# Performance work log

Hardware: AMD Instinct MI355X
Metric: run time of the kernel (lower is better)

## Reference

```python
import jax, jax.numpy as jnp
import numpy as np

N = 100_000          # nodes
E = 1_600_000        # edges (avg degree 16)
NODE_SCA, NODE_VEC = 4, 3
EDGE_SCA, EDGE_VEC = 6, 3
OUT_SCA, OUT_VEC = 16, 16
CUTOFF = 10.0
EPS = 1e-6
SLOPE_VN = 0.2       # VNLeakyReLU negative slope (SurfGen default)
SLOPE_SCA = 0.01     # nn.LeakyReLU default


def setup_inputs() -> dict:
    key = jax.random.key(0)
    ks = jax.random.split(key, 22)
    rn = lambda k, s: jax.random.normal(k, s, dtype=jnp.float32)
    return {
        # forward args
        'node_sca': rn(ks[0], (N, NODE_SCA)),
        'node_vec': rn(ks[1], (N, NODE_VEC, 3)),
        'edge_sca': rn(ks[2], (E, EDGE_SCA)),
        'edge_vec': rn(ks[3], (E, EDGE_VEC, 3)),
        'gds_dist': jax.random.uniform(ks[4], (E,), dtype=jnp.float32) * 12.0,
        'edge_index': jax.random.randint(ks[5], (2, E), 0, N),
        # message projections (Linear weights stored [in,out])
        'W_nss': rn(ks[6], (NODE_SCA, OUT_SCA)) * 0.3, 'b_nss': rn(ks[7], (OUT_SCA,)) * 0.1,
        'W_ess': rn(ks[8], (EDGE_SCA, OUT_SCA)) * 0.3, 'b_ess': rn(ks[9], (OUT_SCA,)) * 0.1,
        'W_nsv': rn(ks[10], (NODE_SCA, OUT_SCA)) * 0.3, 'b_nsv': rn(ks[11], (OUT_SCA,)) * 0.1,
        'W_esv': rn(ks[12], (EDGE_SCA, OUT_SCA)) * 0.3, 'b_esv': rn(ks[13], (OUT_SCA,)) * 0.1,
        'W_nvv': rn(ks[14], (NODE_VEC, OUT_VEC)) * 0.3,   # VNLinear (no bias)
        'W_evv': rn(ks[15], (EDGE_VEC, OUT_VEC)) * 0.3,
        # GVPerceptronVN(16,16,16,16): GVLinear (dim_hid = 16) + VN LeakyReLU
        'W_lv':  rn(ks[16], (OUT_VEC, OUT_VEC)) * 0.25,   # lin_vector   (no bias)
        'W_lv2': rn(ks[17], (OUT_VEC, OUT_VEC)) * 0.25,   # lin_vector2  (no bias)
        'W_ls':  rn(ks[18], (OUT_VEC + OUT_SCA, OUT_SCA)) * 0.25,  # lin_scalar (no bias)
        'W_gate': rn(ks[19], (OUT_SCA, OUT_VEC)) * 0.25, 'b_gate': rn(ks[20], (OUT_VEC,)) * 0.1,
        'W_dir': rn(ks[21], (OUT_VEC, OUT_VEC)) * 0.25,   # VNLeakyReLU direction (no bias)
    }


def vn_linear(x, W):
    # x: [n, c_in, 3], W: [c_in, c_out] -> [n, c_out, 3]
    return jnp.einsum('nci,co->noi', x, W)


def reference(node_sca, node_vec, edge_sca, edge_vec, gds_dist, edge_index,
              W_nss, b_nss, W_ess, b_ess, W_nsv, b_nsv, W_esv, b_esv,
              W_nvv, W_evv, W_lv, W_lv2, W_ls, W_gate, b_gate, W_dir):
    src = edge_index[0]
    num_nodes = node_sca.shape[0]

    # cosine cutoff coefficient
    coeff = 0.5 * (jnp.cos(gds_dist * (jnp.pi / CUTOFF)) + 1.0)
    coeff = coeff * (gds_dist <= CUTOFF) * (gds_dist >= 0.0)  # [E]

    # scalar message: gather node proj, mix with edge proj, cutoff-weight
    node_ss = node_sca @ W_nss + b_nss                          # [N,16]
    edge_ss = edge_sca @ W_ess + b_ess                          # [E,16]
    msg_sca = node_ss[src] * edge_ss * coeff[:, None]           # [E,16]

    # vector message
    node_vv = vn_linear(node_vec, W_nvv)                        # [N,16,3]
    edge_vv = vn_linear(edge_vec, W_evv)                        # [E,16,3]
    node_sv = node_sca @ W_nsv + b_nsv                          # [N,16]
    edge_sv = edge_sca @ W_esv + b_esv                          # [E,16]
    msg_vec = (node_vv[src] * edge_sv[:, :, None]
               + node_sv[src][:, :, None] * edge_vv) * coeff[:, None, None]  # [E,16,3]

    # scatter_sum into source nodes (matches original's edge_index[0])
    aggr_sca = jax.ops.segment_sum(msg_sca, src, num_segments=num_nodes)  # [N,16]
    aggr_vec = jax.ops.segment_sum(msg_vec, src, num_segments=num_nodes)  # [N,16,3]

    # --- GVPerceptronVN: GVLinear ---
    v_inter = vn_linear(aggr_vec, W_lv)                          # [N,16,3]
    v_norm = jnp.sqrt(jnp.sum(v_inter * v_inter, axis=-1))       # [N,16]
    out_sca = jnp.concatenate([v_norm, aggr_sca], axis=-1) @ W_ls  # [N,16]
    out_vec = vn_linear(v_inter, W_lv2)                          # [N,16,3]
    gate = jax.nn.sigmoid(out_sca @ W_gate + b_gate)[:, :, None]
    out_vec = gate * out_vec

    # --- VNLeakyReLU on vectors ---
    d = vn_linear(out_vec, W_dir)                                # [N,16,3]
    dot = jnp.sum(out_vec * d, axis=-1, keepdims=True)
    mask = (dot >= 0).astype(out_vec.dtype)
    d_norm_sq = jnp.sum(d * d, axis=-1, keepdims=True)
    out_vec = SLOPE_VN * out_vec + (1.0 - SLOPE_VN) * (
        mask * out_vec + (1.0 - mask) * (out_vec - (dot / (d_norm_sq + EPS)) * d))

    # LeakyReLU on scalars
    out_sca = jnp.where(out_sca >= 0, out_sca, SLOPE_SCA * out_sca)
    return out_sca, out_vec
```

## Files before the change

kernel.cpp:

```cpp
#include <hip/hip_runtime.h>
#include <hip/hip_fp16.h>
#include <math.h>

#define CUTOFF_F 10.0f
#define PI_OVER_CUTOFF 0.31415926535897931f
#define KCAP 32

__global__ __launch_bounds__(256) void bucket_scatter(
    const float* __restrict__ gds,
    const int* __restrict__ eidx,
    const float* __restrict__ edge_sca,
    const float* __restrict__ edge_vec,
    int* __restrict__ count,
    __half* __restrict__ bucket,
    float* __restrict__ aggr,
    int E)
{
    int e = blockIdx.x * 256 + threadIdx.x;
    if (e >= E) return;

    float d = gds[e];
    if (d < 0.0f || d > CUTOFF_F) return;

    float c = 0.5f * (__cosf(d * PI_OVER_CUTOFF) + 1.0f);
    int src = eidx[e];
    const float* es = edge_sca + (size_t)e * 6;
    const float* ev = edge_vec + (size_t)e * 9;

    float f[16];
#pragma unroll
    for (int i = 0; i < 6; ++i) f[i] = c * es[i];
    f[6] = c;
#pragma unroll
    for (int i = 0; i < 9; ++i) f[7 + i] = c * ev[i];

    int slot = atomicAdd(&count[src], 1);
    if (slot < KCAP) {
        union { __half h[16]; uint4 u[2]; } pk;
#pragma unroll
        for (int i = 0; i < 16; ++i) pk.h[i] = __float2half(f[i]);
        uint4* pb = (uint4*)(bucket + ((size_t)src * KCAP + slot) * 16);
        pb[0] = pk.u[0];
        pb[1] = pk.u[1];
    } else {
        float* base = aggr + (size_t)src * 16;
#pragma unroll
        for (int i = 0; i < 16; ++i) atomicAdd(base + i, f[i]);
    }
}

__global__ __launch_bounds__(256) void edge_aggregate(
    const float* __restrict__ edge_sca, const float* __restrict__ edge_vec,
    const float* __restrict__ gds, const int* __restrict__ eidx,
    float* __restrict__ aggr, int E)
{
    int e = blockIdx.x * blockDim.x + threadIdx.x;
    if (e >= E) return;
    int src = eidx[e];
    float d = gds[e];
    float coeff = 0.0f;
    if (d >= 0.0f && d <= CUTOFF_F)
        coeff = 0.5f * (__cosf(d * PI_OVER_CUTOFF) + 1.0f);
    float* base = aggr + (size_t)src * 16;
    const float* es = edge_sca + (size_t)e * 6;
    const float* ev = edge_vec + (size_t)e * 9;
#pragma unroll
    for (int c = 0; c < 6; ++c) atomicAdd(base + c, coeff * es[c]);
    atomicAdd(base + 6, coeff);
#pragma unroll
    for (int k = 0; k < 9; ++k) atomicAdd(base + 7 + k, coeff * ev[k]);
}

__global__ __launch_bounds__(256) void node_fused(
    const float* __restrict__ node_sca,
    const float* __restrict__ node_vec,
    const int* __restrict__ count,
    const __half* __restrict__ payload,
    const float* __restrict__ aggr,
    const float* __restrict__ W_nss, const float* __restrict__ b_nss,
    const float* __restrict__ W_ess, const float* __restrict__ b_ess,
    const float* __restrict__ W_nsv, const float* __restrict__ b_nsv,
    const float* __restrict__ W_esv, const float* __restrict__ b_esv,
    const float* __restrict__ W_nvv, const float* __restrict__ W_evv,
    const float* __restrict__ W_lv,  const float* __restrict__ W_lv2,
    const float* __restrict__ W_ls,
    const float* __restrict__ W_gate, const float* __restrict__ b_gate,
    const float* __restrict__ W_dir,
    float* __restrict__ out,
    int N, int mode)
{
    __shared__ float sW_nss[64],  sb_nss[16];
    __shared__ float sW_ess[96],  sb_ess[16];
    __shared__ float sW_nsv[64],  sb_nsv[16];
    __shared__ float sW_esv[96],  sb_esv[16];
    __shared__ float sW_nvv[48],  sW_evv[48];
    __shared__ float sW_lv[256],  sW_lv2[256];
    __shared__ float sW_ls[512];
    __shared__ float sW_gate[256], sb_gate[16];
    __shared__ float sW_dir[256];

    __shared__ float s_in  [16 * 33];
    __shared__ float s_avec[16 * 49];
    __shared__ float s_cat [16 * 33];
    __shared__ float s_vint[16 * 49];
    __shared__ float s_osca[16 * 17];
    __shared__ float s_ovec[16 * 49];

    const int t = threadIdx.x;
    {
        for (int i = t; i < 64;  i += 256) { sW_nss[i] = W_nss[i]; sW_nsv[i] = W_nsv[i]; }
        for (int i = t; i < 96;  i += 256) { sW_ess[i] = W_ess[i]; sW_esv[i] = W_esv[i]; }
        for (int i = t; i < 48;  i += 256) { sW_nvv[i] = W_nvv[i]; sW_evv[i] = W_evv[i]; }
        for (int i = t; i < 256; i += 256) {
            sW_lv[i]   = W_lv[i];
            sW_lv2[i]  = W_lv2[i];
            sW_gate[i] = W_gate[i];
            sW_dir[i]  = W_dir[i];
        }
        for (int i = t; i < 512; i += 256) sW_ls[i] = W_ls[i];
        if (t < 16) {
            sb_nss[t]  = b_nss[t];
            sb_ess[t]  = b_ess[t];
            sb_nsv[t]  = b_nsv[t];
            sb_esv[t]  = b_esv[t];
            sb_gate[t] = b_gate[t];
        }
    }

    const int slot = t >> 4;
    const int o    = t & 15;
    const int n    = blockIdx.x * 16 + slot;
    const bool valid = (n < N);

    if (valid) {
        if (o < 4) s_in[slot * 33 + o]     = node_sca[(size_t)n * 4 + o];
        if (o < 9) s_in[slot * 33 + 4 + o] = node_vec[(size_t)n * 9 + o];
    }

    if (mode == 1) {
        float acc[8] = {0.f, 0.f, 0.f, 0.f, 0.f, 0.f, 0.f, 0.f};
        const int h  = o & 1;
        const int sg = o >> 1;
        if (valid) {
            int cnt = count[n];
            if (cnt > KCAP) cnt = KCAP;
            const uint4* pu = (const uint4*)payload + (size_t)n * (KCAP * 2);
#pragma unroll
            for (int k = 0; k < 4; ++k) {
                int s = sg + 8 * k;
                if (s < cnt) {
                    uint4 v = pu[o + 16 * k];
                    const __half2* hp = (const __half2*)&v;
#pragma unroll
                    for (int j = 0; j < 4; ++j) {
                        float2 f2 = __half22float2(hp[j]);
                        acc[2 * j]     += f2.x;
                        acc[2 * j + 1] += f2.y;
                    }
                }
            }
        }
#pragma unroll
        for (int m = 2; m <= 8; m <<= 1) {
#pragma unroll
            for (int j = 0; j < 8; ++j)
                acc[j] += __shfl_xor(acc[j], m, 16);
        }
        if (valid && o < 2) {
#pragma unroll
            for (int j = 0; j < 8; ++j)
                s_in[slot * 33 + 13 + 8 * h + j] =
                    acc[j] + aggr[(size_t)n * 16 + 8 * h + j];
        }
    } else {
        if (valid) s_in[slot * 33 + 13 + o] = aggr[(size_t)n * 16 + o];
    }
    __syncthreads();

    const float* in = s_in + slot * 33;

    float nss = sb_nss[o], nsv = sb_nsv[o];
#pragma unroll
    for (int c = 0; c < 4; ++c) {
        float x = in[c];
        nss += x * sW_nss[c * 16 + o];
        nsv += x * sW_nsv[c * 16 + o];
    }
    float nvv0 = 0.f, nvv1 = 0.f, nvv2 = 0.f;
#pragma unroll
    for (int c = 0; c < 3; ++c) {
        float w = sW_nvv[c * 16 + o];
        nvv0 += in[4 + c * 3 + 0] * w;
        nvv1 += in[4 + c * 3 + 1] * w;
        nvv2 += in[4 + c * 3 + 2] * w;
    }
    float cc = in[19];
    float es = cc * sb_ess[o], ev = cc * sb_esv[o];
#pragma unroll
    for (int c = 0; c < 6; ++c) {
        float a = in[13 + c];
        es += a * sW_ess[c * 16 + o];
        ev += a * sW_esv[c * 16 + o];
    }
    float EV0 = 0.f, EV1 = 0.f, EV2 = 0.f;
#pragma unroll
    for (int c = 0; c < 3; ++c) {
        float w = sW_evv[c * 16 + o];
        EV0 += in[20 + c * 3 + 0] * w;
        EV1 += in[20 + c * 3 + 1] * w;
        EV2 += in[20 + c * 3 + 2] * w;
    }

    float asca = nss * es;
    float av0 = nvv0 * ev + nsv * EV0;
    float av1 = nvv1 * ev + nsv * EV1;
    float av2 = nvv2 * ev + nsv * EV2;
    s_avec[slot * 49 + o * 3 + 0] = av0;
    s_avec[slot * 49 + o * 3 + 1] = av1;
    s_avec[slot * 49 + o * 3 + 2] = av2;
    s_cat[slot * 33 + 16 + o] = asca;
    __syncthreads();

    float vi0 = 0.f, vi1 = 0.f, vi2 = 0.f;
#pragma unroll
    for (int c = 0; c < 16; ++c) {
        float w = sW_lv[c * 16 + o];
        const float* a = &s_avec[slot * 49 + c * 3];
        vi0 += a[0] * w; vi1 += a[1] * w; vi2 += a[2] * w;
    }
    float vnorm = sqrtf(vi0 * vi0 + vi1 * vi1 + vi2 * vi2);
    s_vint[slot * 49 + o * 3 + 0] = vi0;
    s_vint[slot * 49 + o * 3 + 1] = vi1;
    s_vint[slot * 49 + o * 3 + 2] = vi2;
    s_cat[slot * 33 + o] = vnorm;
    __syncthreads();

    float osca = 0.f;
#pragma unroll
    for (int c = 0; c < 32; ++c)
        osca += s_cat[slot * 33 + c] * sW_ls[c * 16 + o];
    float ov0 = 0.f, ov1 = 0.f, ov2 = 0.f;
#pragma unroll
    for (int c = 0; c < 16; ++c) {
        float w = sW_lv2[c * 16 + o];
        const float* a = &s_vint[slot * 49 + c * 3];
        ov0 += a[0] * w; ov1 += a[1] * w; ov2 += a[2] * w;
    }
    s_osca[slot * 17 + o] = osca;
    __syncthreads();

    float g = sb_gate[o];
#pragma unroll
    for (int c = 0; c < 16; ++c)
        g += s_osca[slot * 17 + c] * sW_gate[c * 16 + o];
    g = 1.0f / (1.0f + __expf(-g));
    ov0 *= g; ov1 *= g; ov2 *= g;
    s_ovec[slot * 49 + o * 3 + 0] = ov0;
    s_ovec[slot * 49 + o * 3 + 1] = ov1;
    s_ovec[slot * 49 + o * 3 + 2] = ov2;
    __syncthreads();

    float dv0 = 0.f, dv1 = 0.f, dv2 = 0.f;
#pragma unroll
    for (int c = 0; c < 16; ++c) {
        float w = sW_dir[c * 16 + o];
        const float* a = &s_ovec[slot * 49 + c * 3];
        dv0 += a[0] * w; dv1 += a[1] * w; dv2 += a[2] * w;
    }
    float dot = ov0 * dv0 + ov1 * dv1 + ov2 * dv2;
    if (dot < 0.0f) {
        float dn = dv0 * dv0 + dv1 * dv1 + dv2 * dv2;
        float f = 0.8f * dot / (dn + 1e-6f);
        ov0 -= f * dv0; ov1 -= f * dv1; ov2 -= f * dv2;
    }

    if (valid) {
        float so = (osca >= 0.0f) ? osca : 0.01f * osca;
        out[(size_t)n * 16 + o] = so;
        size_t vb = (size_t)N * 16 + (size_t)n * 48 + (size_t)o * 3;
        out[vb + 0] = ov0;
        out[vb + 1] = ov1;
        out[vb + 2] = ov2;
    }
}

extern "C" void kernel_launch(void* const* d_in, const int* in_sizes, int n_in,
                              void* d_out, int out_size, void* d_ws, size_t ws_size,
                              hipStream_t stream)
{
    const float* node_sca = (const float*)d_in[0];
    const float* node_vec = (const float*)d_in[1];
    const float* edge_sca = (const float*)d_in[2];
    const float* edge_vec = (const float*)d_in[3];
    const float* gds      = (const float*)d_in[4];
    const int*   eidx     = (const int*)d_in[5];

    const int N = in_sizes[0] / 4;
    const int E = in_sizes[4];

    int*    count  = (int*)d_ws;
    float*  aggr   = (float*)(count + N);
    __half* bucket = (__half*)(aggr + (size_t)N * 16);
    size_t  hdr    = (size_t)N * 4 + (size_t)N * 64;
    size_t  need   = hdr + (size_t)N * KCAP * 16 * sizeof(__half);

    if (ws_size >= need) {
        hipMemsetAsync(count, 0, hdr, stream);
        bucket_scatter<<<(E + 255) / 256, 256, 0, stream>>>(
            gds, eidx, edge_sca, edge_vec, count, bucket, aggr, E);
        node_fused<<<(N + 15) / 16, 256, 0, stream>>>(
            node_sca, node_vec, count, bucket, aggr,
            (const float*)d_in[6],  (const float*)d_in[7],
            (const float*)d_in[8],  (const float*)d_in[9],
            (const float*)d_in[10], (const float*)d_in[11],
            (const float*)d_in[12], (const float*)d_in[13],
            (const float*)d_in[14], (const float*)d_in[15],
            (const float*)d_in[16], (const float*)d_in[17],
            (const float*)d_in[18],
            (const float*)d_in[19], (const float*)d_in[20],
            (const float*)d_in[21],
            (float*)d_out, N, 1);
        return;
    }

    size_t zb = hdr;
    if (zb > ws_size) zb = ws_size;
    hipMemsetAsync(count, 0, zb, stream);
    edge_aggregate<<<(E + 255) / 256, 256, 0, stream>>>(
        edge_sca, edge_vec, gds, eidx, aggr, E);
    node_fused<<<(N + 15) / 16, 256, 0, stream>>>(
        node_sca, node_vec, count, bucket, aggr,
        (const float*)d_in[6],  (const float*)d_in[7],
        (const float*)d_in[8],  (const float*)d_in[9],
        (const float*)d_in[10], (const float*)d_in[11],
        (const float*)d_in[12], (const float*)d_in[13],
        (const float*)d_in[14], (const float*)d_in[15],
        (const float*)d_in[16], (const float*)d_in[17],
        (const float*)d_in[18],
        (const float*)d_in[19], (const float*)d_in[20],
        (const float*)d_in[21],
        (float*)d_out, N, 0);
}
```

Measured before the change: 289.1 us.

## Fuse memset, edge scatter and node stage into one cooperative kernel

Replaces the memset, edge bucket-scatter kernel and node kernel with a single cooperative kernel launched on 1024 blocks. The phases are separated by grid-wide syncs, and the loops are grid-strided over edges and node tiles. The aim is to remove launch and inter-kernel gap overhead and to load the weights into shared memory only once per block. In exchange, a fixed grid size may limit parallelism in the scatter phase, and grid syncs add their own cost. If the cooperative launch fails, the code falls back to the previous path.

```diff
diff --git a/kernel.cpp b/kernel.cpp
--- a/kernel.cpp
+++ b/kernel.cpp
@@ -1,10 +1,271 @@
 #include <hip/hip_runtime.h>
+#include <hip/hip_cooperative_groups.h>
 #include <hip/hip_fp16.h>
 #include <math.h>
+
+namespace cg = cooperative_groups;
 
 #define CUTOFF_F 10.0f
 #define PI_OVER_CUTOFF 0.31415926535897931f
 #define KCAP 32
+
+__global__ __launch_bounds__(256) void fused_all(
+    const float* __restrict__ node_sca,
+    const float* __restrict__ node_vec,
+    const float* __restrict__ edge_sca,
+    const float* __restrict__ edge_vec,
+    const float* __restrict__ gds,
+    const int* __restrict__ eidx,
+    int* __restrict__ count,
+    __half* __restrict__ bucket,
+    float* __restrict__ aggr,
+    const float* __restrict__ W_nss, const float* __restrict__ b_nss,
+    const float* __restrict__ W_ess, const float* __restrict__ b_ess,
+    const float* __restrict__ W_nsv, const float* __restrict__ b_nsv,
+    const float* __restrict__ W_esv, const float* __restrict__ b_esv,
+    const float* __restrict__ W_nvv, const float* __restrict__ W_evv,
+    const float* __restrict__ W_lv,  const float* __restrict__ W_lv2,
+    const float* __restrict__ W_ls,
+    const float* __restrict__ W_gate, const float* __restrict__ b_gate,
+    const float* __restrict__ W_dir,
+    float* __restrict__ out,
+    int N, int E)
+{
+    __shared__ float sW_nss[64],  sb_nss[16];
+    __shared__ float sW_ess[96],  sb_ess[16];
+    __shared__ float sW_nsv[64],  sb_nsv[16];
+    __shared__ float sW_esv[96],  sb_esv[16];
+    __shared__ float sW_nvv[48],  sW_evv[48];
+    __shared__ float sW_lv[256],  sW_lv2[256];
+    __shared__ float sW_ls[512];
+    __shared__ float sW_gate[256], sb_gate[16];
+    __shared__ float sW_dir[256];
+
+    __shared__ float s_in  [16 * 33];
+    __shared__ float s_avec[16 * 49];
+    __shared__ float s_cat [16 * 33];
+    __shared__ float s_vint[16 * 49];
+    __shared__ float s_osca[16 * 17];
+    __shared__ float s_ovec[16 * 49];
+
+    const int t = threadIdx.x;
+    {
+        for (int i = t; i < 64;  i += 256) { sW_nss[i] = W_nss[i]; sW_nsv[i] = W_nsv[i]; }
+        for (int i = t; i < 96;  i += 256) { sW_ess[i] = W_ess[i]; sW_esv[i] = W_esv[i]; }
+        for (int i = t; i < 48;  i += 256) { sW_nvv[i] = W_nvv[i]; sW_evv[i] = W_evv[i]; }
+        for (int i = t; i < 256; i += 256) {
+            sW_lv[i]   = W_lv[i];
+            sW_lv2[i]  = W_lv2[i];
+            sW_gate[i] = W_gate[i];
+            sW_dir[i]  = W_dir[i];
+        }
+        for (int i = t; i < 512; i += 256) sW_ls[i] = W_ls[i];
+        if (t < 16) {
+            sb_nss[t]  = b_nss[t];
+            sb_ess[t]  = b_ess[t];
+            sb_nsv[t]  = b_nsv[t];
+            sb_esv[t]  = b_esv[t];
+            sb_gate[t] = b_gate[t];
+        }
+    }
+
+    {
+        int* z = count;
+        const int total = N * 17;
+        for (int i = blockIdx.x * 256 + t; i < total; i += gridDim.x * 256)
+            z[i] = 0;
+    }
+    cg::this_grid().sync();
+
+    for (int e = blockIdx.x * 256 + t; e < E; e += gridDim.x * 256) {
+        float d = gds[e];
+        if (d < 0.0f || d > CUTOFF_F) continue;
+
+        float c = 0.5f * (__cosf(d * PI_OVER_CUTOFF) + 1.0f);
+        int src = eidx[e];
+        const float* es = edge_sca + (size_t)e * 6;
+        const float* ev = edge_vec + (size_t)e * 9;
+
+        float f[16];
+#pragma unroll
+        for (int i = 0; i < 6; ++i) f[i] = c * es[i];
+        f[6] = c;
+#pragma unroll
+        for (int i = 0; i < 9; ++i) f[7 + i] = c * ev[i];
+
+        int sl = atomicAdd(&count[src], 1);
+        if (sl < KCAP) {
+            union { __half h[16]; uint4 u[2]; } pk;
+#pragma unroll
+            for (int i = 0; i < 16; ++i) pk.h[i] = __float2half(f[i]);
+            uint4* pb = (uint4*)(bucket + ((size_t)src * KCAP + sl) * 16);
+            pb[0] = pk.u[0];
+            pb[1] = pk.u[1];
+        } else {
+            float* base = aggr + (size_t)src * 16;
+#pragma unroll
+            for (int i = 0; i < 16; ++i) atomicAdd(base + i, f[i]);
+        }
+    }
+    cg::this_grid().sync();
+
+    const int slot = t >> 4;
+    const int o    = t & 15;
+    const int h    = o & 1;
+    const int sg   = o >> 1;
+    const int nTiles = (N + 15) / 16;
+
+    for (int tile = blockIdx.x; tile < nTiles; tile += gridDim.x) {
+        const int n = tile * 16 + slot;
+        const bool valid = (n < N);
+
+        if (valid) {
+            if (o < 4) s_in[slot * 33 + o]     = node_sca[(size_t)n * 4 + o];
+            if (o < 9) s_in[slot * 33 + 4 + o] = node_vec[(size_t)n * 9 + o];
+        }
+
+        float acc[8] = {0.f, 0.f, 0.f, 0.f, 0.f, 0.f, 0.f, 0.f};
+        if (valid) {
+            int cnt = count[n];
+            if (cnt > KCAP) cnt = KCAP;
+            const uint4* pu = (const uint4*)bucket + (size_t)n * (KCAP * 2);
+#pragma unroll
+            for (int k = 0; k < 4; ++k) {
+                int s = sg + 8 * k;
+                if (s < cnt) {
+                    uint4 v = pu[o + 16 * k];
+                    const __half2* hp = (const __half2*)&v;
+#pragma unroll
+                    for (int j = 0; j < 4; ++j) {
+                        float2 f2 = __half22float2(hp[j]);
+                        acc[2 * j]     += f2.x;
+                        acc[2 * j + 1] += f2.y;
+                    }
+                }
+            }
+        }
+#pragma unroll
+        for (int m = 2; m <= 8; m <<= 1) {
+#pragma unroll
+            for (int j = 0; j < 8; ++j)
+                acc[j] += __shfl_xor(acc[j], m, 16);
+        }
+        if (valid && o < 2) {
+#pragma unroll
+            for (int j = 0; j < 8; ++j)
+                s_in[slot * 33 + 13 + 8 * h + j] =
+                    acc[j] + aggr[(size_t)n * 16 + 8 * h + j];
+        }
+        __syncthreads();
+
+        const float* in = s_in + slot * 33;
+
+        float nss = sb_nss[o], nsv = sb_nsv[o];
+#pragma unroll
+        for (int c = 0; c < 4; ++c) {
+            float x = in[c];
+            nss += x * sW_nss[c * 16 + o];
+            nsv += x * sW_nsv[c * 16 + o];
+        }
+        float nvv0 = 0.f, nvv1 = 0.f, nvv2 = 0.f;
+#pragma unroll
+        for (int c = 0; c < 3; ++c) {
+            float w = sW_nvv[c * 16 + o];
+            nvv0 += in[4 + c * 3 + 0] * w;
+            nvv1 += in[4 + c * 3 + 1] * w;
+            nvv2 += in[4 + c * 3 + 2] * w;
+        }
+        float cc = in[19];
+        float es = cc * sb_ess[o], ev = cc * sb_esv[o];
+#pragma unroll
+        for (int c = 0; c < 6; ++c) {
+            float a = in[13 + c];
+            es += a * sW_ess[c * 16 + o];
+            ev += a * sW_esv[c * 16 + o];
+        }
+        float EV0 = 0.f, EV1 = 0.f, EV2 = 0.f;
+#pragma unroll
+        for (int c = 0; c < 3; ++c) {
+            float w = sW_evv[c * 16 + o];
+            EV0 += in[20 + c * 3 + 0] * w;
+            EV1 += in[20 + c * 3 + 1] * w;
+            EV2 += in[20 + c * 3 + 2] * w;
+        }
+
+        float asca = nss * es;
+        float av0 = nvv0 * ev + nsv * EV0;
+        float av1 = nvv1 * ev + nsv * EV1;
+        float av2 = nvv2 * ev + nsv * EV2;
+        s_avec[slot * 49 + o * 3 + 0] = av0;
+        s_avec[slot * 49 + o * 3 + 1] = av1;
+        s_avec[slot * 49 + o * 3 + 2] = av2;
+        s_cat[slot * 33 + 16 + o] = asca;
+        __syncthreads();
+
+        float vi0 = 0.f, vi1 = 0.f, vi2 = 0.f;
+#pragma unroll
+        for (int c = 0; c < 16; ++c) {
+            float w = sW_lv[c * 16 + o];
+            const float* a = &s_avec[slot * 49 + c * 3];
+            vi0 += a[0] * w; vi1 += a[1] * w; vi2 += a[2] * w;
+        }
+        float vnorm = sqrtf(vi0 * vi0 + vi1 * vi1 + vi2 * vi2);
+        s_vint[slot * 49 + o * 3 + 0] = vi0;
+        s_vint[slot * 49 + o * 3 + 1] = vi1;
+        s_vint[slot * 49 + o * 3 + 2] = vi2;
+        s_cat[slot * 33 + o] = vnorm;
+        __syncthreads();
+
+        float osca = 0.f;
+#pragma unroll
+        for (int c = 0; c < 32; ++c)
+            osca += s_cat[slot * 33 + c] * sW_ls[c * 16 + o];
+        float ov0 = 0.f, ov1 = 0.f, ov2 = 0.f;
+#pragma unroll
+        for (int c = 0; c < 16; ++c) {
+            float w = sW_lv2[c * 16 + o];
+            const float* a = &s_vint[slot * 49 + c * 3];
+            ov0 += a[0] * w; ov1 += a[1] * w; ov2 += a[2] * w;
+        }
+        s_osca[slot * 17 + o] = osca;
+        __syncthreads();
+
+        float g = sb_gate[o];
+#pragma unroll
+        for (int c = 0; c < 16; ++c)
+            g += s_osca[slot * 17 + c] * sW_gate[c * 16 + o];
+        g = 1.0f / (1.0f + __expf(-g));
+        ov0 *= g; ov1 *= g; ov2 *= g;
+        s_ovec[slot * 49 + o * 3 + 0] = ov0;
+        s_ovec[slot * 49 + o * 3 + 1] = ov1;
+        s_ovec[slot * 49 + o * 3 + 2] = ov2;
+        __syncthreads();
+
+        float dv0 = 0.f, dv1 = 0.f, dv2 = 0.f;
+#pragma unroll
+        for (int c = 0; c < 16; ++c) {
+            float w = sW_dir[c * 16 + o];
+            const float* a = &s_ovec[slot * 49 + c * 3];
+            dv0 += a[0] * w; dv1 += a[1] * w; dv2 += a[2] * w;
+        }
+        float dot = ov0 * dv0 + ov1 * dv1 + ov2 * dv2;
+        if (dot < 0.0f) {
+            float dn = dv0 * dv0 + dv1 * dv1 + dv2 * dv2;
+            float fr = 0.8f * dot / (dn + 1e-6f);
+            ov0 -= fr * dv0; ov1 -= fr * dv1; ov2 -= fr * dv2;
+        }
+
+        if (valid) {
+            float so = (osca >= 0.0f) ? osca : 0.01f * osca;
+            out[(size_t)n * 16 + o] = so;
+            size_t vb = (size_t)N * 16 + (size_t)n * 48 + (size_t)o * 3;
+            out[vb + 0] = ov0;
+            out[vb + 1] = ov1;
+            out[vb + 2] = ov2;
+        }
+        __syncthreads();
+    }
+}
 
 __global__ __launch_bounds__(256) void bucket_scatter(
     const float* __restrict__ gds,
@@ -305,6 +566,40 @@
     size_t  need   = hdr + (size_t)N * KCAP * 16 * sizeof(__half);
 
     if (ws_size >= need) {
+        const float* p_Wnss = (const float*)d_in[6];
+        const float* p_bnss = (const float*)d_in[7];
+        const float* p_Wess = (const float*)d_in[8];
+        const float* p_bess = (const float*)d_in[9];
+        const float* p_Wnsv = (const float*)d_in[10];
+        const float* p_bnsv = (const float*)d_in[11];
+        const float* p_Wesv = (const float*)d_in[12];
+        const float* p_besv = (const float*)d_in[13];
+        const float* p_Wnvv = (const float*)d_in[14];
+        const float* p_Wevv = (const float*)d_in[15];
+        const float* p_Wlv  = (const float*)d_in[16];
+        const float* p_Wlv2 = (const float*)d_in[17];
+        const float* p_Wls  = (const float*)d_in[18];
+        const float* p_Wgt  = (const float*)d_in[19];
+        const float* p_bgt  = (const float*)d_in[20];
+        const float* p_Wdir = (const float*)d_in[21];
+        float* p_out = (float*)d_out;
+        int nN = N, nE = E;
+
+        void* kargs[] = {
+            (void*)&node_sca, (void*)&node_vec, (void*)&edge_sca,
+            (void*)&edge_vec, (void*)&gds, (void*)&eidx,
+            (void*)&count, (void*)&bucket, (void*)&aggr,
+            (void*)&p_Wnss, (void*)&p_bnss, (void*)&p_Wess, (void*)&p_bess,
+            (void*)&p_Wnsv, (void*)&p_bnsv, (void*)&p_Wesv, (void*)&p_besv,
+            (void*)&p_Wnvv, (void*)&p_Wevv, (void*)&p_Wlv, (void*)&p_Wlv2,
+            (void*)&p_Wls, (void*)&p_Wgt, (void*)&p_bgt, (void*)&p_Wdir,
+            (void*)&p_out, (void*)&nN, (void*)&nE
+        };
+
+        hipError_t err = hipLaunchCooperativeKernel(
+            (const void*)fused_all, dim3(1024), dim3(256), kargs, 0, stream);
+        if (err == hipSuccess) return;
+
         hipMemsetAsync(count, 0, hdr, stream);
         bucket_scatter<<<(E + 255) / 256, 256, 0, stream>>>(
             gds, eidx, edge_sca, edge_vec, count, bucket, aggr, E);
```

Measured after the change: 532.2 us. 1.84x slower.

## Add overflow flag, nontemporal bucket stores, and persistent node kernel grid

Applied to the files above, without the earlier changes.

The scatter kernel now writes bucket entries with nontemporal stores and sets a global flag whenever any node exceeds its bucket capacity. The node kernel reads that flag once per block and skips reading the dense aggregate array when no overflow happened. The node kernel also becomes a grid-stride loop over a fixed number of blocks, so shared-memory weight staging is paid once per block rather than once per 16 nodes. The risks are an extra barrier per tile iteration and possibly lower occupancy from the capped grid.

```diff
diff --git a/kernel.cpp b/kernel.cpp
--- a/kernel.cpp
+++ b/kernel.cpp
@@ -5,6 +5,8 @@
 #define CUTOFF_F 10.0f
 #define PI_OVER_CUTOFF 0.31415926535897931f
 #define KCAP 32
+
+typedef unsigned int uint32x4 __attribute__((ext_vector_type(4)));
 
 __global__ __launch_bounds__(256) void bucket_scatter(
     const float* __restrict__ gds,
@@ -12,6 +14,7 @@
     const float* __restrict__ edge_sca,
     const float* __restrict__ edge_vec,
     int* __restrict__ count,
+    int* __restrict__ flag,
     __half* __restrict__ bucket,
     float* __restrict__ aggr,
     int E)
@@ -36,13 +39,14 @@
 
     int slot = atomicAdd(&count[src], 1);
     if (slot < KCAP) {
-        union { __half h[16]; uint4 u[2]; } pk;
+        union { __half h[16]; uint32x4 u[2]; } pk;
 #pragma unroll
         for (int i = 0; i < 16; ++i) pk.h[i] = __float2half(f[i]);
-        uint4* pb = (uint4*)(bucket + ((size_t)src * KCAP + slot) * 16);
-        pb[0] = pk.u[0];
-        pb[1] = pk.u[1];
+        uint32x4* pb = (uint32x4*)(bucket + ((size_t)src * KCAP + slot) * 16);
+        __builtin_nontemporal_store(pk.u[0], pb);
+        __builtin_nontemporal_store(pk.u[1], pb + 1);
     } else {
+        flag[0] = 1;
         float* base = aggr + (size_t)src * 16;
 #pragma unroll
         for (int i = 0; i < 16; ++i) atomicAdd(base + i, f[i]);
@@ -75,6 +79,7 @@
     const float* __restrict__ node_sca,
     const float* __restrict__ node_vec,
     const int* __restrict__ count,
+    const int* __restrict__ flag,
     const __half* __restrict__ payload,
     const float* __restrict__ aggr,
     const float* __restrict__ W_nss, const float* __restrict__ b_nss,
@@ -105,6 +110,7 @@
     __shared__ float s_vint[16 * 49];
     __shared__ float s_osca[16 * 17];
     __shared__ float s_ovec[16 * 49];
+    __shared__ int   s_flag;
 
     const int t = threadIdx.x;
     {
@@ -125,162 +131,176 @@
             sb_esv[t]  = b_esv[t];
             sb_gate[t] = b_gate[t];
         }
+        if (t == 0) s_flag = flag[0];
     }
+    __syncthreads();
 
     const int slot = t >> 4;
     const int o    = t & 15;
-    const int n    = blockIdx.x * 16 + slot;
-    const bool valid = (n < N);
-
-    if (valid) {
-        if (o < 4) s_in[slot * 33 + o]     = node_sca[(size_t)n * 4 + o];
-        if (o < 9) s_in[slot * 33 + 4 + o] = node_vec[(size_t)n * 9 + o];
-    }
-
-    if (mode == 1) {
-        float acc[8] = {0.f, 0.f, 0.f, 0.f, 0.f, 0.f, 0.f, 0.f};
-        const int h  = o & 1;
-        const int sg = o >> 1;
+    const int h    = o & 1;
+    const int sg   = o >> 1;
+    const int useOvf = s_flag;
+    const int nTiles = (N + 15) / 16;
+
+    for (int tile = blockIdx.x; tile < nTiles; tile += gridDim.x) {
+        const int n = tile * 16 + slot;
+        const bool valid = (n < N);
+
         if (valid) {
-            int cnt = count[n];
-            if (cnt > KCAP) cnt = KCAP;
-            const uint4* pu = (const uint4*)payload + (size_t)n * (KCAP * 2);
-#pragma unroll
-            for (int k = 0; k < 4; ++k) {
-                int s = sg + 8 * k;
-                if (s < cnt) {
-                    uint4 v = pu[o + 16 * k];
-                    const __half2* hp = (const __half2*)&v;
-#pragma unroll
-                    for (int j = 0; j < 4; ++j) {
-                        float2 f2 = __half22float2(hp[j]);
-                        acc[2 * j]     += f2.x;
-                        acc[2 * j + 1] += f2.y;
+            if (o < 4) s_in[slot * 33 + o]     = node_sca[(size_t)n * 4 + o];
+            if (o < 9) s_in[slot * 33 + 4 + o] = node_vec[(size_t)n * 9 + o];
+        }
+
+        if (mode == 1) {
+            float acc[8] = {0.f, 0.f, 0.f, 0.f, 0.f, 0.f, 0.f, 0.f};
+            if (valid) {
+                int cnt = count[n];
+                if (cnt > KCAP) cnt = KCAP;
+                const uint4* pu = (const uint4*)payload + (size_t)n * (KCAP * 2);
+#pragma unroll
+                for (int k = 0; k < 4; ++k) {
+                    int s = sg + 8 * k;
+                    if (s < cnt) {
+                        uint4 v = pu[o + 16 * k];
+                        const __half2* hp = (const __half2*)&v;
+#pragma unroll
+                        for (int j = 0; j < 4; ++j) {
+                            float2 f2 = __half22float2(hp[j]);
+                            acc[2 * j]     += f2.x;
+                            acc[2 * j + 1] += f2.y;
+                        }
                     }
                 }
             }
-        }
-#pragma unroll
-        for (int m = 2; m <= 8; m <<= 1) {
-#pragma unroll
-            for (int j = 0; j < 8; ++j)
-                acc[j] += __shfl_xor(acc[j], m, 16);
-        }
-        if (valid && o < 2) {
-#pragma unroll
-            for (int j = 0; j < 8; ++j)
-                s_in[slot * 33 + 13 + 8 * h + j] =
-                    acc[j] + aggr[(size_t)n * 16 + 8 * h + j];
-        }
-    } else {
-        if (valid) s_in[slot * 33 + 13 + o] = aggr[(size_t)n * 16 + o];
-    }
-    __syncthreads();
-
-    const float* in = s_in + slot * 33;
-
-    float nss = sb_nss[o], nsv = sb_nsv[o];
-#pragma unroll
-    for (int c = 0; c < 4; ++c) {
-        float x = in[c];
-        nss += x * sW_nss[c * 16 + o];
-        nsv += x * sW_nsv[c * 16 + o];
-    }
-    float nvv0 = 0.f, nvv1 = 0.f, nvv2 = 0.f;
-#pragma unroll
-    for (int c = 0; c < 3; ++c) {
-        float w = sW_nvv[c * 16 + o];
-        nvv0 += in[4 + c * 3 + 0] * w;
-        nvv1 += in[4 + c * 3 + 1] * w;
-        nvv2 += in[4 + c * 3 + 2] * w;
-    }
-    float cc = in[19];
-    float es = cc * sb_ess[o], ev = cc * sb_esv[o];
-#pragma unroll
-    for (int c = 0; c < 6; ++c) {
-        float a = in[13 + c];
-        es += a * sW_ess[c * 16 + o];
-        ev += a * sW_esv[c * 16 + o];
-    }
-    float EV0 = 0.f, EV1 = 0.f, EV2 = 0.f;
-#pragma unroll
-    for (int c = 0; c < 3; ++c) {
-        float w = sW_evv[c * 16 + o];
-        EV0 += in[20 + c * 3 + 0] * w;
-        EV1 += in[20 + c * 3 + 1] * w;
-        EV2 += in[20 + c * 3 + 2] * w;
-    }
-
-    float asca = nss * es;
-    float av0 = nvv0 * ev + nsv * EV0;
-    float av1 = nvv1 * ev + nsv * EV1;
-    float av2 = nvv2 * ev + nsv * EV2;
-    s_avec[slot * 49 + o * 3 + 0] = av0;
-    s_avec[slot * 49 + o * 3 + 1] = av1;
-    s_avec[slot * 49 + o * 3 + 2] = av2;
-    s_cat[slot * 33 + 16 + o] = asca;
-    __syncthreads();
-
-    float vi0 = 0.f, vi1 = 0.f, vi2 = 0.f;
-#pragma unroll
-    for (int c = 0; c < 16; ++c) {
-        float w = sW_lv[c * 16 + o];
-        const float* a = &s_avec[slot * 49 + c * 3];
-        vi0 += a[0] * w; vi1 += a[1] * w; vi2 += a[2] * w;
-    }
-    float vnorm = sqrtf(vi0 * vi0 + vi1 * vi1 + vi2 * vi2);
-    s_vint[slot * 49 + o * 3 + 0] = vi0;
-    s_vint[slot * 49 + o * 3 + 1] = vi1;
-    s_vint[slot * 49 + o * 3 + 2] = vi2;
-    s_cat[slot * 33 + o] = vnorm;
-    __syncthreads();
-
-    float osca = 0.f;
-#pragma unroll
-    for (int c = 0; c < 32; ++c)
-        osca += s_cat[slot * 33 + c] * sW_ls[c * 16 + o];
-    float ov0 = 0.f, ov1 = 0.f, ov2 = 0.f;
-#pragma unroll
-    for (int c = 0; c < 16; ++c) {
-        float w = sW_lv2[c * 16 + o];
-        const float* a = &s_vint[slot * 49 + c * 3];
-        ov0 += a[0] * w; ov1 += a[1] * w; ov2 += a[2] * w;
-    }
-    s_osca[slot * 17 + o] = osca;
-    __syncthreads();
-
-    float g = sb_gate[o];
-#pragma unroll
-    for (int c = 0; c < 16; ++c)
-        g += s_osca[slot * 17 + c] * sW_gate[c * 16 + o];
-    g = 1.0f / (1.0f + __expf(-g));
-    ov0 *= g; ov1 *= g; ov2 *= g;
-    s_ovec[slot * 49 + o * 3 + 0] = ov0;
-    s_ovec[slot * 49 + o * 3 + 1] = ov1;
-    s_ovec[slot * 49 + o * 3 + 2] = ov2;
-    __syncthreads();
-
-    float dv0 = 0.f, dv1 = 0.f, dv2 = 0.f;
-#pragma unroll
-    for (int c = 0; c < 16; ++c) {
-        float w = sW_dir[c * 16 + o];
-        const float* a = &s_ovec[slot * 49 + c * 3];
-        dv0 += a[0] * w; dv1 += a[1] * w; dv2 += a[2] * w;
-    }
-    float dot = ov0 * dv0 + ov1 * dv1 + ov2 * dv2;
-    if (dot < 0.0f) {
-        float dn = dv0 * dv0 + dv1 * dv1 + dv2 * dv2;
-        float f = 0.8f * dot / (dn + 1e-6f);
-        ov0 -= f * dv0; ov1 -= f * dv1; ov2 -= f * dv2;
-    }
-
-    if (valid) {
-        float so = (osca >= 0.0f) ? osca : 0.01f * osca;
-        out[(size_t)n * 16 + o] = so;
-        size_t vb = (size_t)N * 16 + (size_t)n * 48 + (size_t)o * 3;
-        out[vb + 0] = ov0;
-        out[vb + 1] = ov1;
-        out[vb + 2] = ov2;
+#pragma unroll
+            for (int m = 2; m <= 8; m <<= 1) {
+#pragma unroll
+                for (int j = 0; j < 8; ++j)
+                    acc[j] += __shfl_xor(acc[j], m, 16);
+            }
+            if (valid && o < 2) {
+                if (useOvf) {
+#pragma unroll
+                    for (int j = 0; j < 8; ++j)
+                        s_in[slot * 33 + 13 + 8 * h + j] =
+                            acc[j] + aggr[(size_t)n * 16 + 8 * h + j];
+                } else {
+#pragma unroll
+                    for (int j = 0; j < 8; ++j)
+                        s_in[slot * 33 + 13 + 8 * h + j] = acc[j];
+                }
+            }
+        } else {
+            if (valid) s_in[slot * 33 + 13 + o] = aggr[(size_t)n * 16 + o];
+        }
+        __syncthreads();
+
+        const float* in = s_in + slot * 33;
+
+        float nss = sb_nss[o], nsv = sb_nsv[o];
+#pragma unroll
+        for (int c = 0; c < 4; ++c) {
+            float x = in[c];
+            nss += x * sW_nss[c * 16 + o];
+            nsv += x * sW_nsv[c * 16 + o];
+        }
+        float nvv0 = 0.f, nvv1 = 0.f, nvv2 = 0.f;
+#pragma unroll
+        for (int c = 0; c < 3; ++c) {
+            float w = sW_nvv[c * 16 + o];
+            nvv0 += in[4 + c * 3 + 0] * w;
+            nvv1 += in[4 + c * 3 + 1] * w;
+            nvv2 += in[4 + c * 3 + 2] * w;
+        }
+        float cc = in[19];
+        float es = cc * sb_ess[o], ev = cc * sb_esv[o];
+#pragma unroll
+        for (int c = 0; c < 6; ++c) {
+            float a = in[13 + c];
+            es += a * sW_ess[c * 16 + o];
+            ev += a * sW_esv[c * 16 + o];
+        }
+        float EV0 = 0.f, EV1 = 0.f, EV2 = 0.f;
+#pragma unroll
+        for (int c = 0; c < 3; ++c) {
+            float w = sW_evv[c * 16 + o];
+            EV0 += in[20 + c * 3 + 0] * w;
+            EV1 += in[20 + c * 3 + 1] * w;
+            EV2 += in[20 + c * 3 + 2] * w;
+        }
+
+        float asca = nss * es;
+        float av0 = nvv0 * ev + nsv * EV0;
+        float av1 = nvv1 * ev + nsv * EV1;
+        float av2 = nvv2 * ev + nsv * EV2;
+        s_avec[slot * 49 + o * 3 + 0] = av0;
+        s_avec[slot * 49 + o * 3 + 1] = av1;
+        s_avec[slot * 49 + o * 3 + 2] = av2;
+        s_cat[slot * 33 + 16 + o] = asca;
+        __syncthreads();
+
+        float vi0 = 0.f, vi1 = 0.f, vi2 = 0.f;
+#pragma unroll
+        for (int c = 0; c < 16; ++c) {
+            float w = sW_lv[c * 16 + o];
+            const float* a = &s_avec[slot * 49 + c * 3];
+            vi0 += a[0] * w; vi1 += a[1] * w; vi2 += a[2] * w;
+        }
+        float vnorm = sqrtf(vi0 * vi0 + vi1 * vi1 + vi2 * vi2);
+        s_vint[slot * 49 + o * 3 + 0] = vi0;
+        s_vint[slot * 49 + o * 3 + 1] = vi1;
+        s_vint[slot * 49 + o * 3 + 2] = vi2;
+        s_cat[slot * 33 + o] = vnorm;
+        __syncthreads();
+
+        float osca = 0.f;
+#pragma unroll
+        for (int c = 0; c < 32; ++c)
+            osca += s_cat[slot * 33 + c] * sW_ls[c * 16 + o];
+        float ov0 = 0.f, ov1 = 0.f, ov2 = 0.f;
+#pragma unroll
+        for (int c = 0; c < 16; ++c) {
+            float w = sW_lv2[c * 16 + o];
+            const float* a = &s_vint[slot * 49 + c * 3];
+            ov0 += a[0] * w; ov1 += a[1] * w; ov2 += a[2] * w;
+        }
+        s_osca[slot * 17 + o] = osca;
+        __syncthreads();
+
+        float g = sb_gate[o];
+#pragma unroll
+        for (int c = 0; c < 16; ++c)
+            g += s_osca[slot * 17 + c] * sW_gate[c * 16 + o];
+        g = 1.0f / (1.0f + __expf(-g));
+        ov0 *= g; ov1 *= g; ov2 *= g;
+        s_ovec[slot * 49 + o * 3 + 0] = ov0;
+        s_ovec[slot * 49 + o * 3 + 1] = ov1;
+        s_ovec[slot * 49 + o * 3 + 2] = ov2;
+        __syncthreads();
+
+        float dv0 = 0.f, dv1 = 0.f, dv2 = 0.f;
+#pragma unroll
+        for (int c = 0; c < 16; ++c) {
+            float w = sW_dir[c * 16 + o];
+            const float* a = &s_ovec[slot * 49 + c * 3];
+            dv0 += a[0] * w; dv1 += a[1] * w; dv2 += a[2] * w;
+        }
+        float dot = ov0 * dv0 + ov1 * dv1 + ov2 * dv2;
+        if (dot < 0.0f) {
+            float dn = dv0 * dv0 + dv1 * dv1 + dv2 * dv2;
+            float fr = 0.8f * dot / (dn + 1e-6f);
+            ov0 -= fr * dv0; ov1 -= fr * dv1; ov2 -= fr * dv2;
+        }
+
+        if (valid) {
+            float so = (osca >= 0.0f) ? osca : 0.01f * osca;
+            out[(size_t)n * 16 + o] = so;
+            size_t vb = (size_t)N * 16 + (size_t)n * 48 + (size_t)o * 3;
+            out[vb + 0] = ov0;
+            out[vb + 1] = ov1;
+            out[vb + 2] = ov2;
+        }
+        __syncthreads();
     }
 }
 
@@ -299,17 +319,22 @@
     const int E = in_sizes[4];
 
     int*    count  = (int*)d_ws;
-    float*  aggr   = (float*)(count + N);
+    int*    flag   = count + N;
+    float*  aggr   = (float*)(flag + 16);
     __half* bucket = (__half*)(aggr + (size_t)N * 16);
-    size_t  hdr    = (size_t)N * 4 + (size_t)N * 64;
+    size_t  hdr    = (size_t)N * 4 + 64 + (size_t)N * 64;
     size_t  need   = hdr + (size_t)N * KCAP * 16 * sizeof(__half);
 
+    const int nTiles = (N + 15) / 16;
+    int nodeGrid = 1280;
+    if (nodeGrid > nTiles) nodeGrid = nTiles;
+
     if (ws_size >= need) {
-        hipMemsetAsync(count, 0, hdr, stream);
+        (void)hipMemsetAsync(count, 0, hdr, stream);
         bucket_scatter<<<(E + 255) / 256, 256, 0, stream>>>(
-            gds, eidx, edge_sca, edge_vec, count, bucket, aggr, E);
-        node_fused<<<(N + 15) / 16, 256, 0, stream>>>(
-            node_sca, node_vec, count, bucket, aggr,
+            gds, eidx, edge_sca, edge_vec, count, flag, bucket, aggr, E);
+        node_fused<<<nodeGrid, 256, 0, stream>>>(
+            node_sca, node_vec, count, flag, bucket, aggr,
             (const float*)d_in[6],  (const float*)d_in[7],
             (const float*)d_in[8],  (const float*)d_in[9],
             (const float*)d_in[10], (const float*)d_in[11],
@@ -325,11 +350,11 @@
 
     size_t zb = hdr;
     if (zb > ws_size) zb = ws_size;
-    hipMemsetAsync(count, 0, zb, stream);
+    (void)hipMemsetAsync(count, 0, zb, stream);
     edge_aggregate<<<(E + 255) / 256, 256, 0, stream>>>(
         edge_sca, edge_vec, gds, eidx, aggr, E);
-    node_fused<<<(N + 15) / 16, 256, 0, stream>>>(
-        node_sca, node_vec, count, bucket, aggr,
+    node_fused<<<nodeGrid, 256, 0, stream>>>(
+        node_sca, node_vec, count, flag, bucket, aggr,
         (const float*)d_in[6],  (const float*)d_in[7],
         (const float*)d_in[8],  (const float*)d_in[9],
         (const float*)d_in[10], (const float*)d_in[11],
```

New measurement: 333.4 us. 1.15x slower.
